# Optimization experiments

Measured on AMD Instinct MI355X. Metric: run time of the kernel, lower is better.

## Reference

```python
import jax, jax.numpy as jnp
import numpy as np

B, N, DIM, H = 2, 4096, 512, 8
DH = DIM // H  # head dim = 64


def setup_inputs() -> dict:
    key = jax.random.key(0)
    kx, kw, kb = jax.random.split(key, 3)
    x = jax.random.normal(kx, (B, N, DIM), dtype=jnp.float32)
    W = jax.random.normal(kw, (DIM, 3 * DIM), dtype=jnp.float32) / np.sqrt(DIM)
    b = jax.random.normal(kb, (3 * DIM,), dtype=jnp.float32) * 0.02
    return {"x": x, "W": W, "b": b}


def reference(x, W, b):
    Bx, n, d = x.shape
    qvk = x @ W + b  # [B, n, 3*dim]
    # torch.chunk order in source: q, v, k
    q, v, k = jnp.split(qvk, 3, axis=-1)

    def heads(t):  # [B, n, dim] -> [B, h, n, dh]
        return t.reshape(Bx, n, H, DH).transpose(0, 2, 1, 3)

    q, v, k = heads(q), heads(v), heads(k)
    # full (non-fused) attention: materializes [B, h, n, n] scores
    scale = jnp.einsum('bhqd,bhkd->bhqk', q, k) / jnp.sqrt(jnp.float32(DH))
    atn = jax.nn.softmax(scale, axis=-1)
    out = jnp.einsum('bhqk,bhkd->bhqd', atn, v)  # [B, h, n, dh]
    # concat_head: [B, h, n, dh] -> [B, n, h*dh]
    out = out.transpose(0, 2, 1, 3).reshape(Bx, n, H * DH)
    return out
```

## Files before the change

### kernel.cpp

```cpp
#include <hip/hip_runtime.h>
#include <hip/hip_bf16.h>
#include <math.h>

#define BB    2
#define NN    4096
#define DIM   512
#define NH    8
#define DH    64
#define NC    1536
#define MM    (BB*NN)

typedef __bf16 bf16x8 __attribute__((ext_vector_type(8)));
typedef __bf16 bf16x4 __attribute__((ext_vector_type(4)));
typedef float  f32x4  __attribute__((ext_vector_type(4)));

#define QSCALE 0.18033688011112042f

__device__ __forceinline__ int swz(int c) { return c ^ (((c >> 3) ^ (c >> 6)) & 7); }

__device__ __forceinline__ void gl_lds16(const __hip_bfloat16* g, __bf16* l) {
    __builtin_amdgcn_global_load_lds(
        (const __attribute__((address_space(1))) unsigned int*)g,
        (__attribute__((address_space(3))) unsigned int*)l, 16, 0, 0);
}

__device__ __forceinline__ int sniff(const unsigned short* x) {
    unsigned short v = x[2 * (threadIdx.x & 63)];
    int e = (v >> 7) & 0xFF;
    unsigned long long m = __ballot(e >= 110 && e <= 140);
    return __popcll(m) >= 48;
}

__global__ __launch_bounds__(256) void prep_kernel(
    const void* __restrict__ xin, const void* __restrict__ win,
    const void* __restrict__ bin,
    __hip_bfloat16* __restrict__ Xb, __hip_bfloat16* __restrict__ WT,
    float* __restrict__ Bf)
{
    int bfmode = sniff((const unsigned short*)xin);
    int bid = blockIdx.x;
    if (bid < 2048) {
        int i = (bid * 256 + threadIdx.x) * 8;
        if (bfmode) {
            *(bf16x8*)(Xb + i) = *(const bf16x8*)((const __hip_bfloat16*)xin + i);
        } else {
            const float* xf = (const float*)xin + i;
            bf16x8 v;
            for (int j = 0; j < 8; j++) v[j] = (__bf16)xf[j];
            *(bf16x8*)(Xb + i) = v;
        }
    } else if (bid < 2048 + 3072) {
        int i = (bid - 2048) * 256 + threadIdx.x;
        int n = i >> 9, k = i & 511;
        float v = bfmode ? __bfloat162float(((const __hip_bfloat16*)win)[k * NC + n])
                         : ((const float*)win)[k * NC + n];
        WT[i] = __float2bfloat16(v);
    } else {
        int i = (bid - 2048 - 3072) * 256 + threadIdx.x;
        if (i < NC)
            Bf[i] = bfmode ? __bfloat162float(((const __hip_bfloat16*)bin)[i])
                           : ((const float*)bin)[i];
    }
}

__global__ __launch_bounds__(256, 3) void qkv_gemm(
    const __hip_bfloat16* __restrict__ X,
    const __hip_bfloat16* __restrict__ WT,
    const float* __restrict__ Bf,
    __hip_bfloat16* __restrict__ Qb,
    __hip_bfloat16* __restrict__ Kb,
    __hip_bfloat16* __restrict__ Vt)
{
    __shared__ __align__(16) __bf16 Xs[2][4096];
    __shared__ __align__(16) __bf16 Ws[2][4096];

    int wave = threadIdx.x >> 6, lane = threadIdx.x & 63;
    int lane16 = lane & 15, quad = lane >> 4;
    int bm = blockIdx.x / 12, bn = blockIdx.x % 12;
    int m0b = bm * 128, n0b = bn * 128;
    int wm = wave >> 1, wn = wave & 1;
    int m0 = m0b + wm * 64, n0 = n0b + wn * 64;

    int xgo[2], sbase[2];
    for (int j = 0; j < 2; j++) {
        int p = (wave * 2 + j) * 64 + lane;
        int g = swz(p);
        xgo[j] = (g >> 2) * DIM + (g & 3) * 8;
        sbase[j] = (wave * 2 + j) * 512;
    }
    int aoff[4], boff[4];
    for (int mi = 0; mi < 4; mi++) {
        int c = (wm * 64 + mi * 16 + lane16) * 4 + quad;
        aoff[mi] = swz(c) * 8;
    }
    for (int ni = 0; ni < 4; ni++) {
        int c = (wn * 64 + ni * 16 + lane16) * 4 + quad;
        boff[ni] = swz(c) * 8;
    }

    const __hip_bfloat16* Xg = X  + (size_t)m0b * DIM;
    const __hip_bfloat16* Wg = WT + (size_t)n0b * DIM;

    for (int j = 0; j < 2; j++) {
        gl_lds16(Xg + xgo[j], &Xs[0][sbase[j]]);
        gl_lds16(Wg + xgo[j], &Ws[0][sbase[j]]);
    }
    __syncthreads();

    f32x4 acc[4][4] = {};
    for (int k0 = 0; k0 < DIM; k0 += 32) {
        int cur = (k0 >> 5) & 1, nbuf = cur ^ 1;
        int k1 = (k0 + 32) & (DIM - 1);
        for (int j = 0; j < 2; j++) {
            gl_lds16(Xg + k1 + xgo[j], &Xs[nbuf][sbase[j]]);
            gl_lds16(Wg + k1 + xgo[j], &Ws[nbuf][sbase[j]]);
        }
        bf16x8 a[4], b[4];
        for (int mi = 0; mi < 4; mi++) a[mi] = *(const bf16x8*)&Xs[cur][aoff[mi]];
        for (int ni = 0; ni < 4; ni++) b[ni] = *(const bf16x8*)&Ws[cur][boff[ni]];
        for (int mi = 0; mi < 4; mi++)
            for (int ni = 0; ni < 4; ni++)
                acc[mi][ni] = __builtin_amdgcn_mfma_f32_16x16x32_bf16(a[mi], b[ni], acc[mi][ni], 0, 0, 0);
        __syncthreads();
    }

    for (int mi = 0; mi < 4; mi++) {
        for (int ni = 0; ni < 4; ni++) {
            int col = n0 + ni * 16 + lane16;
            float bv = Bf[col];
            int sec = col >> 9;
            int c   = col & 511;
            int h   = c >> 6, d = c & 63;
            for (int r = 0; r < 4; r++) {
                int m = m0 + mi * 16 + quad * 4 + r;
                int bidx = m >> 12, nrow = m & 4095;
                int bh = bidx * 8 + h;
                float v = acc[mi][ni][r] + bv;
                if (sec == 0)
                    Qb[((size_t)bh * NN + nrow) * DH + d] = __float2bfloat16(v * QSCALE);
                else if (sec == 2)
                    Kb[((size_t)bh * NN + nrow) * DH + d] = __float2bfloat16(v);
                else
                    Vt[((size_t)bh * DH + d) * NN + nrow] = __float2bfloat16(v);
            }
        }
    }
}

__global__ __launch_bounds__(256, 2) void attn_kernel(
    const __hip_bfloat16* __restrict__ Qb,
    const __hip_bfloat16* __restrict__ Kb,
    const __hip_bfloat16* __restrict__ Vt,
    void* __restrict__ OutV,
    const unsigned short* __restrict__ xs)
{
    __shared__ __align__(16) __bf16 Kst[2][4096];
    __shared__ __align__(16) __bf16 Vst[2][4096];
    __shared__ __align__(16) __bf16 lds_p[4][32][72];

    int bfmode = sniff(xs);
    int wave = threadIdx.x >> 6, lane = threadIdx.x & 63;
    int lane16 = lane & 15, quad = lane >> 4;
    int i = blockIdx.x;
    int bh = i & 15;
    int qt = i >> 4;
    int q0 = qt * 128 + wave * 32;

    const __hip_bfloat16* Qh = Qb + (size_t)bh * NN * DH;
    const __hip_bfloat16* Kh = Kb + (size_t)bh * NN * DH;
    const __hip_bfloat16* Vh = Vt + (size_t)bh * DH * NN;

    bf16x8 aq[2][2];
    for (int rf = 0; rf < 2; rf++)
        for (int kc = 0; kc < 2; kc++)
            aq[rf][kc] = *(const bf16x8*)(Qh + (size_t)(q0 + rf * 16 + lane16) * DH + kc * 32 + quad * 8);

    int kgo[2], vgo[2], sbase[2];
    for (int j = 0; j < 2; j++) {
        int p = (wave * 2 + j) * 64 + lane;
        int g = swz(p);
        kgo[j] = (g >> 3) * DH + (g & 7) * 8;
        vgo[j] = (g >> 3) * NN + (g & 7) * 8;
        sbase[j] = (wave * 2 + j) * 512;
    }
    int koff[4][2], voff[4][2];
    for (int kf = 0; kf < 4; kf++)
        for (int kc = 0; kc < 2; kc++) {
            int c = (4 * lane16 + kf) * 8 + kc * 4 + quad;
            koff[kf][kc] = swz(c) * 8;
        }
    for (int dt = 0; dt < 4; dt++)
        for (int kc = 0; kc < 2; kc++) {
            int c = (dt * 16 + lane16) * 8 + kc * 4 + quad;
            voff[dt][kc] = swz(c) * 8;
        }

    for (int j = 0; j < 2; j++) {
        gl_lds16(Kh + kgo[j], &Kst[0][sbase[j]]);
        gl_lds16(Vh + vgo[j], &Vst[0][sbase[j]]);
    }
    __syncthreads();

    bf16x8 vones;
    for (int j = 0; j < 8; j++) vones[j] = (__bf16)1.0f;
    f32x4 o[2][4] = {};
    f32x4 ol[2] = {};

    for (int k0 = 0; k0 < NN; k0 += 64) {
        int cur = (k0 >> 6) & 1, nb = cur ^ 1;
        int k1 = (k0 + 64) & (NN - 1);
        for (int j = 0; j < 2; j++) {
            gl_lds16(Kh + (size_t)k1 * DH + kgo[j], &Kst[nb][sbase[j]]);
            gl_lds16(Vh + k1 + vgo[j], &Vst[nb][sbase[j]]);
        }

        bf16x8 kb[4][2], vb[4][2];
        for (int kf = 0; kf < 4; kf++)
            for (int kc = 0; kc < 2; kc++)
                kb[kf][kc] = *(const bf16x8*)&Kst[cur][koff[kf][kc]];
        for (int dt = 0; dt < 4; dt++)
            for (int kc = 0; kc < 2; kc++)
                vb[dt][kc] = *(const bf16x8*)&Vst[cur][voff[dt][kc]];

        f32x4 s[2][4];
        for (int rf = 0; rf < 2; rf++)
            for (int kf = 0; kf < 4; kf++) {
                f32x4 t = {};
                t = __builtin_amdgcn_mfma_f32_16x16x32_bf16(aq[rf][0], kb[kf][0], t, 0, 0, 0);
                t = __builtin_amdgcn_mfma_f32_16x16x32_bf16(aq[rf][1], kb[kf][1], t, 0, 0, 0);
                s[rf][kf] = t;
            }

        for (int rf = 0; rf < 2; rf++)
            for (int r = 0; r < 4; r++) {
                bf16x4 pk;
                pk[0] = (__bf16)__builtin_amdgcn_exp2f(fminf(s[rf][0][r], 60.0f));
                pk[1] = (__bf16)__builtin_amdgcn_exp2f(fminf(s[rf][1][r], 60.0f));
                pk[2] = (__bf16)__builtin_amdgcn_exp2f(fminf(s[rf][2][r], 60.0f));
                pk[3] = (__bf16)__builtin_amdgcn_exp2f(fminf(s[rf][3][r], 60.0f));
                *(bf16x4*)(&lds_p[wave][rf * 16 + quad * 4 + r][4 * lane16]) = pk;
            }
        bf16x8 pa[2][2];
        for (int rf = 0; rf < 2; rf++)
            for (int kc = 0; kc < 2; kc++)
                pa[rf][kc] = *(const bf16x8*)(&lds_p[wave][rf * 16 + lane16][kc * 32 + quad * 8]);

        for (int rf = 0; rf < 2; rf++) {
            for (int dt = 0; dt < 4; dt++) {
                o[rf][dt] = __builtin_amdgcn_mfma_f32_16x16x32_bf16(pa[rf][0], vb[dt][0], o[rf][dt], 0, 0, 0);
                o[rf][dt] = __builtin_amdgcn_mfma_f32_16x16x32_bf16(pa[rf][1], vb[dt][1], o[rf][dt], 0, 0, 0);
            }
            ol[rf] = __builtin_amdgcn_mfma_f32_16x16x32_bf16(pa[rf][0], vones, ol[rf], 0, 0, 0);
            ol[rf] = __builtin_amdgcn_mfma_f32_16x16x32_bf16(pa[rf][1], vones, ol[rf], 0, 0, 0);
        }

        __syncthreads();
    }

    for (int rf = 0; rf < 2; rf++) {
        float rinv[4];
        for (int r = 0; r < 4; r++) rinv[r] = 1.0f / ol[rf][r];
        for (int dt = 0; dt < 4; dt++)
            for (int r = 0; r < 4; r++)
                lds_p[wave][rf * 16 + quad * 4 + r][dt * 16 + lane16] =
                    (__bf16)(o[rf][dt][r] * rinv[r]);
    }
    int bidx = bh >> 3, h = bh & 7;
    for (int rr = 0; rr < 4; rr++) {
        int row = rr * 8 + (lane >> 3);
        int nrow = q0 + row;
        int c0 = (lane & 7) * 8;
        bf16x8 vv = *(const bf16x8*)(&lds_p[wave][row][c0]);
        size_t base = ((size_t)bidx * NN + nrow) * DIM + h * 64 + c0;
        if (bfmode) {
            *(bf16x8*)((__hip_bfloat16*)OutV + base) = vv;
        } else {
            float* op = (float*)OutV + base;
            f32x4 f0, f1;
            for (int j = 0; j < 4; j++) { f0[j] = (float)vv[j]; f1[j] = (float)vv[4 + j]; }
            *(f32x4*)op = f0;
            *(f32x4*)(op + 4) = f1;
        }
    }
}

extern "C" void kernel_launch(void* const* d_in, const int* in_sizes, int n_in,
                              void* d_out, int out_size, void* d_ws, size_t ws_size,
                              hipStream_t stream) {
    char* ws = (char*)d_ws;
    __hip_bfloat16* WT = (__hip_bfloat16*)ws;
    __hip_bfloat16* Xb = WT + (size_t)NC * DIM;
    float* Bf = (float*)(Xb + (size_t)MM * DIM);
    __hip_bfloat16* Qb = (__hip_bfloat16*)(Bf + NC);
    __hip_bfloat16* Kb = Qb + (size_t)BB * NH * NN * DH;
    __hip_bfloat16* Vt = Kb + (size_t)BB * NH * NN * DH;

    prep_kernel<<<2048 + 3072 + 6, 256, 0, stream>>>(d_in[0], d_in[1], d_in[2], Xb, WT, Bf);
    qkv_gemm<<<(MM / 128) * (NC / 128), 256, 0, stream>>>(Xb, WT, Bf, Qb, Kb, Vt);
    attn_kernel<<<512, 256, 0, stream>>>(Qb, Kb, Vt, d_out, (const unsigned short*)d_in[0]);
}
```

Before: 204.2 us.

## Tile W transpose, stage V-transpose epilogue in LDS, double attention rows per wave

The W transpose in the prep kernel now goes through a shared-memory tile, so both the reads and the writes are coalesced. The bf16 path skips the X copy, and the GEMM reads the input directly. The GEMM's V section now writes its transposed output through a swizzled LDS staging buffer as 16-byte stores, replacing scattered 2-byte stores. The attention kernel gives each wave 64 query rows instead of 32, which doubles K/V reuse per LDS load but halves the grid to 256 blocks with occupancy of 1. That lower occupancy and the extra register pressure may hurt latency hiding.

```diff
diff --git a/kernel.cpp b/kernel.cpp
--- a/kernel.cpp
+++ b/kernel.cpp
@@ -37,34 +37,44 @@
     __hip_bfloat16* __restrict__ Xb, __hip_bfloat16* __restrict__ WT,
     float* __restrict__ Bf)
 {
+    __shared__ __bf16 tile[64][68];
     int bfmode = sniff((const unsigned short*)xin);
     int bid = blockIdx.x;
+    int t = threadIdx.x;
     if (bid < 2048) {
-        int i = (bid * 256 + threadIdx.x) * 8;
-        if (bfmode) {
-            *(bf16x8*)(Xb + i) = *(const bf16x8*)((const __hip_bfloat16*)xin + i);
-        } else {
-            const float* xf = (const float*)xin + i;
-            bf16x8 v;
-            for (int j = 0; j < 8; j++) v[j] = (__bf16)xf[j];
-            *(bf16x8*)(Xb + i) = v;
-        }
-    } else if (bid < 2048 + 3072) {
-        int i = (bid - 2048) * 256 + threadIdx.x;
-        int n = i >> 9, k = i & 511;
-        float v = bfmode ? __bfloat162float(((const __hip_bfloat16*)win)[k * NC + n])
-                         : ((const float*)win)[k * NC + n];
-        WT[i] = __float2bfloat16(v);
+        if (bfmode) return;
+        int i = (bid * 256 + t) * 8;
+        const float* xf = (const float*)xin + i;
+        bf16x8 v;
+        for (int j = 0; j < 8; j++) v[j] = (__bf16)xf[j];
+        *(bf16x8*)(Xb + i) = v;
+    } else if (bid < 2048 + 192) {
+        int tl = bid - 2048;
+        int kt = tl / 24, nt = tl % 24;
+        int tx = t & 63, tyq = t >> 6;
+        for (int r = 0; r < 16; r++) {
+            int kl = r * 4 + tyq;
+            int gi = (kt * 64 + kl) * NC + nt * 64 + tx;
+            float v = bfmode ? __bfloat162float(((const __hip_bfloat16*)win)[gi])
+                             : ((const float*)win)[gi];
+            tile[kl][tx] = (__bf16)v;
+        }
+        __syncthreads();
+        for (int r = 0; r < 16; r++) {
+            int nl = r * 4 + tyq;
+            WT[(size_t)(nt * 64 + nl) * DIM + kt * 64 + tx] = (__hip_bfloat16)(float)tile[tx][nl];
+        }
     } else {
-        int i = (bid - 2048 - 3072) * 256 + threadIdx.x;
+        int i = (bid - 2048 - 192) * 256 + t;
         if (i < NC)
             Bf[i] = bfmode ? __bfloat162float(((const __hip_bfloat16*)bin)[i])
                            : ((const float*)bin)[i];
     }
 }
 
-__global__ __launch_bounds__(256, 3) void qkv_gemm(
-    const __hip_bfloat16* __restrict__ X,
+__global__ __launch_bounds__(256, 2) void qkv_gemm(
+    const unsigned short* __restrict__ xs,
+    const __hip_bfloat16* __restrict__ Xb,
     const __hip_bfloat16* __restrict__ WT,
     const float* __restrict__ Bf,
     __hip_bfloat16* __restrict__ Qb,
@@ -73,6 +83,10 @@
 {
     __shared__ __align__(16) __bf16 Xs[2][4096];
     __shared__ __align__(16) __bf16 Ws[2][4096];
+    __shared__ __align__(16) __bf16 epi[4][4096];
+
+    int bfmode = sniff(xs);
+    const __hip_bfloat16* X = bfmode ? (const __hip_bfloat16*)xs : Xb;
 
     int wave = threadIdx.x >> 6, lane = threadIdx.x & 63;
     int lane16 = lane & 15, quad = lane >> 4;
@@ -89,14 +103,10 @@
         sbase[j] = (wave * 2 + j) * 512;
     }
     int aoff[4], boff[4];
-    for (int mi = 0; mi < 4; mi++) {
-        int c = (wm * 64 + mi * 16 + lane16) * 4 + quad;
-        aoff[mi] = swz(c) * 8;
-    }
-    for (int ni = 0; ni < 4; ni++) {
-        int c = (wn * 64 + ni * 16 + lane16) * 4 + quad;
-        boff[ni] = swz(c) * 8;
-    }
+    for (int mi = 0; mi < 4; mi++)
+        aoff[mi] = swz((wm * 64 + mi * 16 + lane16) * 4 + quad) * 8;
+    for (int ni = 0; ni < 4; ni++)
+        boff[ni] = swz((wn * 64 + ni * 16 + lane16) * 4 + quad) * 8;
 
     const __hip_bfloat16* Xg = X  + (size_t)m0b * DIM;
     const __hip_bfloat16* Wg = WT + (size_t)n0b * DIM;
@@ -124,30 +134,48 @@
         __syncthreads();
     }
 
-    for (int mi = 0; mi < 4; mi++) {
+    int sec = n0b >> 9;
+    if (sec == 1) {
         for (int ni = 0; ni < 4; ni++) {
-            int col = n0 + ni * 16 + lane16;
-            float bv = Bf[col];
-            int sec = col >> 9;
-            int c   = col & 511;
-            int h   = c >> 6, d = c & 63;
-            for (int r = 0; r < 4; r++) {
-                int m = m0 + mi * 16 + quad * 4 + r;
-                int bidx = m >> 12, nrow = m & 4095;
-                int bh = bidx * 8 + h;
-                float v = acc[mi][ni][r] + bv;
-                if (sec == 0)
-                    Qb[((size_t)bh * NN + nrow) * DH + d] = __float2bfloat16(v * QSCALE);
-                else if (sec == 2)
-                    Kb[((size_t)bh * NN + nrow) * DH + d] = __float2bfloat16(v);
-                else
-                    Vt[((size_t)bh * DH + d) * NN + nrow] = __float2bfloat16(v);
-            }
-        }
-    }
-}
-
-__global__ __launch_bounds__(256, 2) void attn_kernel(
+            int nloc = ni * 16 + lane16;
+            float bv = Bf[n0 + nloc];
+            for (int mi = 0; mi < 4; mi++) {
+                bf16x4 pk;
+                for (int r = 0; r < 4; r++) pk[r] = (__bf16)(acc[mi][ni][r] + bv);
+                int idx = swz(nloc * 8 + mi * 2 + (quad >> 1)) * 8 + (quad & 1) * 4;
+                *(bf16x4*)&epi[wave][idx] = pk;
+            }
+        }
+        int hl = (n0 - 512) >> 6;
+        int bidx = m0b >> 12;
+        int mbase = m0b - bidx * NN + wm * 64;
+        for (int p = 0; p < 8; p++) {
+            int n = p * 8 + (lane >> 3), mc = lane & 7;
+            bf16x8 vv = *(const bf16x8*)&epi[wave][swz(n * 8 + mc) * 8];
+            *(bf16x8*)(Vt + ((size_t)(bidx * 8 + hl) * 64 + n) * NN + mbase + mc * 8) = vv;
+        }
+    } else {
+        bool isQ = (sec == 0);
+        for (int mi = 0; mi < 4; mi++) {
+            for (int ni = 0; ni < 4; ni++) {
+                int col = n0 + ni * 16 + lane16;
+                float bv = Bf[col];
+                int c = col & 511;
+                int h = c >> 6, d = c & 63;
+                for (int r = 0; r < 4; r++) {
+                    int m = m0 + mi * 16 + quad * 4 + r;
+                    int bidx = m >> 12, nrow = m & 4095;
+                    int bh = bidx * 8 + h;
+                    float v = acc[mi][ni][r] + bv;
+                    if (isQ) Qb[((size_t)bh * NN + nrow) * DH + d] = __float2bfloat16(v * QSCALE);
+                    else     Kb[((size_t)bh * NN + nrow) * DH + d] = __float2bfloat16(v);
+                }
+            }
+        }
+    }
+}
+
+__global__ __launch_bounds__(256, 1) void attn_kernel(
     const __hip_bfloat16* __restrict__ Qb,
     const __hip_bfloat16* __restrict__ Kb,
     const __hip_bfloat16* __restrict__ Vt,
@@ -156,7 +184,7 @@
 {
     __shared__ __align__(16) __bf16 Kst[2][4096];
     __shared__ __align__(16) __bf16 Vst[2][4096];
-    __shared__ __align__(16) __bf16 lds_p[4][32][72];
+    __shared__ __align__(16) __bf16 Pp[4][4096];
 
     int bfmode = sniff(xs);
     int wave = threadIdx.x >> 6, lane = threadIdx.x & 63;
@@ -164,16 +192,16 @@
     int i = blockIdx.x;
     int bh = i & 15;
     int qt = i >> 4;
-    int q0 = qt * 128 + wave * 32;
+    int q0w = qt * 256 + wave * 64;
 
     const __hip_bfloat16* Qh = Qb + (size_t)bh * NN * DH;
     const __hip_bfloat16* Kh = Kb + (size_t)bh * NN * DH;
     const __hip_bfloat16* Vh = Vt + (size_t)bh * DH * NN;
 
-    bf16x8 aq[2][2];
-    for (int rf = 0; rf < 2; rf++)
+    bf16x8 aq[4][2];
+    for (int rf = 0; rf < 4; rf++)
         for (int kc = 0; kc < 2; kc++)
-            aq[rf][kc] = *(const bf16x8*)(Qh + (size_t)(q0 + rf * 16 + lane16) * DH + kc * 32 + quad * 8);
+            aq[rf][kc] = *(const bf16x8*)(Qh + (size_t)(q0w + rf * 16 + lane16) * DH + kc * 32 + quad * 8);
 
     int kgo[2], vgo[2], sbase[2];
     for (int j = 0; j < 2; j++) {
@@ -183,17 +211,19 @@
         vgo[j] = (g >> 3) * NN + (g & 7) * 8;
         sbase[j] = (wave * 2 + j) * 512;
     }
-    int koff[4][2], voff[4][2];
+    int koff[4][2], voff[4][2], poffr[4][2], poffw[4][4];
     for (int kf = 0; kf < 4; kf++)
-        for (int kc = 0; kc < 2; kc++) {
-            int c = (4 * lane16 + kf) * 8 + kc * 4 + quad;
-            koff[kf][kc] = swz(c) * 8;
-        }
+        for (int kc = 0; kc < 2; kc++)
+            koff[kf][kc] = swz((4 * lane16 + kf) * 8 + kc * 4 + quad) * 8;
     for (int dt = 0; dt < 4; dt++)
-        for (int kc = 0; kc < 2; kc++) {
-            int c = (dt * 16 + lane16) * 8 + kc * 4 + quad;
-            voff[dt][kc] = swz(c) * 8;
-        }
+        for (int kc = 0; kc < 2; kc++)
+            voff[dt][kc] = swz((dt * 16 + lane16) * 8 + kc * 4 + quad) * 8;
+    for (int rf = 0; rf < 4; rf++) {
+        for (int kc = 0; kc < 2; kc++)
+            poffr[rf][kc] = swz((rf * 16 + lane16) * 8 + kc * 4 + quad) * 8;
+        for (int r = 0; r < 4; r++)
+            poffw[rf][r] = swz((rf * 16 + quad * 4 + r) * 8 + (lane16 >> 1)) * 8 + (lane16 & 1) * 4;
+    }
 
     for (int j = 0; j < 2; j++) {
         gl_lds16(Kh + kgo[j], &Kst[0][sbase[j]]);
@@ -203,8 +233,8 @@
 
     bf16x8 vones;
     for (int j = 0; j < 8; j++) vones[j] = (__bf16)1.0f;
-    f32x4 o[2][4] = {};
-    f32x4 ol[2] = {};
+    f32x4 o[4][4] = {};
+    f32x4 ol[4] = {};
 
     for (int k0 = 0; k0 < NN; k0 += 64) {
         int cur = (k0 >> 6) & 1, nb = cur ^ 1;
@@ -222,8 +252,8 @@
             for (int kc = 0; kc < 2; kc++)
                 vb[dt][kc] = *(const bf16x8*)&Vst[cur][voff[dt][kc]];
 
-        f32x4 s[2][4];
-        for (int rf = 0; rf < 2; rf++)
+        f32x4 s[4][4];
+        for (int rf = 0; rf < 4; rf++)
             for (int kf = 0; kf < 4; kf++) {
                 f32x4 t = {};
                 t = __builtin_amdgcn_mfma_f32_16x16x32_bf16(aq[rf][0], kb[kf][0], t, 0, 0, 0);
@@ -231,21 +261,21 @@
                 s[rf][kf] = t;
             }
 
-        for (int rf = 0; rf < 2; rf++)
+        for (int rf = 0; rf < 4; rf++)
             for (int r = 0; r < 4; r++) {
                 bf16x4 pk;
                 pk[0] = (__bf16)__builtin_amdgcn_exp2f(fminf(s[rf][0][r], 60.0f));
                 pk[1] = (__bf16)__builtin_amdgcn_exp2f(fminf(s[rf][1][r], 60.0f));
                 pk[2] = (__bf16)__builtin_amdgcn_exp2f(fminf(s[rf][2][r], 60.0f));
                 pk[3] = (__bf16)__builtin_amdgcn_exp2f(fminf(s[rf][3][r], 60.0f));
-                *(bf16x4*)(&lds_p[wave][rf * 16 + quad * 4 + r][4 * lane16]) = pk;
-            }
-        bf16x8 pa[2][2];
-        for (int rf = 0; rf < 2; rf++)
+                *(bf16x4*)&Pp[wave][poffw[rf][r]] = pk;
+            }
+        bf16x8 pa[4][2];
+        for (int rf = 0; rf < 4; rf++)
             for (int kc = 0; kc < 2; kc++)
-                pa[rf][kc] = *(const bf16x8*)(&lds_p[wave][rf * 16 + lane16][kc * 32 + quad * 8]);
-
-        for (int rf = 0; rf < 2; rf++) {
+                pa[rf][kc] = *(const bf16x8*)&Pp[wave][poffr[rf][kc]];
+
+        for (int rf = 0; rf < 4; rf++) {
             for (int dt = 0; dt < 4; dt++) {
                 o[rf][dt] = __builtin_amdgcn_mfma_f32_16x16x32_bf16(pa[rf][0], vb[dt][0], o[rf][dt], 0, 0, 0);
                 o[rf][dt] = __builtin_amdgcn_mfma_f32_16x16x32_bf16(pa[rf][1], vb[dt][1], o[rf][dt], 0, 0, 0);
@@ -257,21 +287,22 @@
         __syncthreads();
     }
 
-    for (int rf = 0; rf < 2; rf++) {
+    for (int rf = 0; rf < 4; rf++) {
         float rinv[4];
         for (int r = 0; r < 4; r++) rinv[r] = 1.0f / ol[rf][r];
         for (int dt = 0; dt < 4; dt++)
-            for (int r = 0; r < 4; r++)
-                lds_p[wave][rf * 16 + quad * 4 + r][dt * 16 + lane16] =
-                    (__bf16)(o[rf][dt][r] * rinv[r]);
+            for (int r = 0; r < 4; r++) {
+                int row = rf * 16 + quad * 4 + r;
+                int d = dt * 16 + lane16;
+                int idx = swz(row * 8 + (d >> 3)) * 8 + (d & 7);
+                Pp[wave][idx] = (__bf16)(o[rf][dt][r] * rinv[r]);
+            }
     }
     int bidx = bh >> 3, h = bh & 7;
-    for (int rr = 0; rr < 4; rr++) {
-        int row = rr * 8 + (lane >> 3);
-        int nrow = q0 + row;
-        int c0 = (lane & 7) * 8;
-        bf16x8 vv = *(const bf16x8*)(&lds_p[wave][row][c0]);
-        size_t base = ((size_t)bidx * NN + nrow) * DIM + h * 64 + c0;
+    for (int p = 0; p < 8; p++) {
+        int row = p * 8 + (lane >> 3), mc = lane & 7;
+        bf16x8 vv = *(const bf16x8*)&Pp[wave][swz(row * 8 + mc) * 8];
+        size_t base = ((size_t)bidx * NN + q0w + row) * DIM + h * 64 + mc * 8;
         if (bfmode) {
             *(bf16x8*)((__hip_bfloat16*)OutV + base) = vv;
         } else {
@@ -295,7 +326,8 @@
     __hip_bfloat16* Kb = Qb + (size_t)BB * NH * NN * DH;
     __hip_bfloat16* Vt = Kb + (size_t)BB * NH * NN * DH;
 
-    prep_kernel<<<2048 + 3072 + 6, 256, 0, stream>>>(d_in[0], d_in[1], d_in[2], Xb, WT, Bf);
-    qkv_gemm<<<(MM / 128) * (NC / 128), 256, 0, stream>>>(Xb, WT, Bf, Qb, Kb, Vt);
-    attn_kernel<<<512, 256, 0, stream>>>(Qb, Kb, Vt, d_out, (const unsigned short*)d_in[0]);
-}
+    prep_kernel<<<2048 + 192 + 6, 256, 0, stream>>>(d_in[0], d_in[1], d_in[2], Xb, WT, Bf);
+    qkv_gemm<<<(MM / 128) * (NC / 128), 256, 0, stream>>>(
+        (const unsigned short*)d_in[0], Xb, WT, Bf, Qb, Kb, Vt);
+    attn_kernel<<<256, 256, 0, stream>>>(Qb, Kb, Vt, d_out, (const unsigned short*)d_in[0]);
+}
```

After: 263.6 us. 29.0% more time.
